# Kernel optimization log

Hardware: AMD Instinct MI355X
Metric: run time of the kernel (lower is better)

Reference implementation:

```python
import jax, jax.numpy as jnp
import numpy as np

N = 8192
EPS = 1e-8
RADIUS2 = 0.05 ** 2  # squared neighborhood radius


def setup_inputs() -> dict:
    key = jax.random.key(0)
    ks = jax.random.split(key, 6)
    points = jax.random.uniform(ks[0], (N, 3), dtype=jnp.float32)
    seg_probs = jax.random.uniform(ks[1], (N, 3), dtype=jnp.float32)
    boundary_mask = jax.random.randint(ks[2], (N,), 0, 2) > 0
    head_mask = jax.random.randint(ks[3], (N,), 0, 2) > 0
    pred_mask = jax.random.randint(ks[4], (N,), 0, 2) > 0
    gt_mask = jax.random.randint(ks[5], (N,), 0, 2) > 0
    return {"points": points, "seg_probs": seg_probs,
            "boundary_mask": boundary_mask, "head_mask": head_mask,
            "pred_mask": pred_mask, "gt_mask": gt_mask}


def _ellipsoid_shape_loss(points, mask):
    # masked mean / covariance over head-region points, then eigen ratios
    m = mask.astype(points.dtype)[:, None]  # [N,1]
    n = jnp.sum(m)
    center = jnp.sum(points * m, axis=0) / n
    centered = (points - center) * m  # zero out non-head rows
    cov = centered.T @ centered / n  # [3,3]
    w = jnp.linalg.eigvalsh(cov)  # ascending
    a, b, c = w[2], w[1], w[0]  # descending
    loss = (b / (a + EPS) - 1.0) ** 2 + (c / (a + EPS) - 1.0) ** 2
    return jnp.where(n >= 10, loss, 0.0)


def _size_consistency_loss(pred_mask, gt_mask):
    pv = jnp.sum(pred_mask.astype(jnp.float32))
    gv = jnp.sum(gt_mask.astype(jnp.float32))
    volume_loss = (pv - gv) ** 2
    rel = jnp.abs(pv - gv) / jnp.where(gv > 0, gv, 1.0)
    return jnp.where(gv > 0, volume_loss + 0.5 * rel, volume_loss)


def _surface_smoothness_loss(points, bmask, seg_probs):
    # fused pairwise-distance + masked unbiased variance (replaces O(N) python loop)
    bf = bmask.astype(points.dtype)
    x = seg_probs[:, 2]  # head probability channel
    sq = jnp.sum(points * points, axis=1)  # [N]
    d2 = sq[:, None] + sq[None, :] - 2.0 * (points @ points.T)  # [N,N] squared dists
    vf = (d2 < RADIUS2).astype(points.dtype) * bf[:, None] * bf[None, :]  # valid pairs
    cnt = jnp.sum(vf, axis=1)  # neighbors per boundary point (incl. self)
    sx = vf @ x
    sx2 = vf @ (x * x)
    safe_n = jnp.maximum(cnt, 2.0)
    var = (sx2 - sx * sx / safe_n) / (safe_n - 1.0)  # unbiased, matches torch.var
    include = (cnt > 1.0) & bmask
    ni = jnp.sum(include)
    mean_var = jnp.sum(jnp.where(include, var, 0.0)) / jnp.maximum(ni, 1)
    ok = (jnp.sum(bf) >= 5) & (ni > 0)
    return jnp.where(ok, mean_var, 0.0)


def _connectivity_loss(points, hmask):
    hf = hmask.astype(points.dtype)
    n = jnp.sum(hf)
    center = jnp.sum(points * hf[:, None], axis=0) / n
    d = jnp.linalg.norm(points - center, axis=1)
    mean_d = jnp.sum(d * hf) / n
    var = jnp.sum(hf * (d - mean_d) ** 2) / (n - 1.0)  # unbiased
    maxd = jnp.max(jnp.where(hmask, d, -jnp.inf))
    return jnp.where(n >= 5, var / (maxd + EPS), 0.0)


def reference(points, seg_probs, boundary_mask, head_mask, pred_mask, gt_mask):
    total = (_ellipsoid_shape_loss(points, head_mask)
             + _size_consistency_loss(pred_mask, gt_mask)
             + _surface_smoothness_loss(points, boundary_mask, seg_probs)
             + _connectivity_loss(points, head_mask))
    return total
```

## Files before the change

### kernel.cpp

```cpp
#include <hip/hip_runtime.h>

#define EPSF 1e-8f
#define R2C  0.0025f
#define NJ   32


__device__ inline int read_mask(const void* p, int i, int isInt) {
    if (isInt) return ((const int*)p)[i] != 0;
    return ((const unsigned char*)p)[i] != 0;
}
__device__ inline float wave_sum(float v) {
    #pragma unroll
    for (int o = 32; o > 0; o >>= 1) v += __shfl_down(v, o, 64);
    return v;
}
__device__ inline float wave_max(float v) {
    #pragma unroll
    for (int o = 32; o > 0; o >>= 1) v = fmaxf(v, __shfl_down(v, o, 64));
    return v;
}

__global__ __launch_bounds__(256, 4)
void k_pairs(const float* __restrict__ pts, const float* __restrict__ segp,
             const void* bm, const void* hm, const void* pm, const void* gm,
             float* __restrict__ ws, int n, int nbi) {
    __shared__ float4 t4[256];
    __shared__ float2 tv[256];
    __shared__ int bad[4];
    __shared__ float pacc[8];
    int tid = threadIdx.x, lane = tid & 63;
    int bx = blockIdx.x, c = blockIdx.y;

    if (tid < 4) bad[tid] = 0;
    if (tid < 8) pacc[tid] = 0.f;
    __syncthreads();
    {
        const void* ms[4] = {bm, hm, pm, gm};
        #pragma unroll
        for (int m = 0; m < 4; ++m) {
            unsigned w = ((const unsigned*)ms[m])[tid & 255];
            if (w & 0xFFFFFF00u) atomicOr(&bad[m], 1);
        }
    }
    __syncthreads();

    int i0 = bx*512 + tid, i1 = i0 + 256;
    int ic0 = min(i0, n-1), ic1 = min(i1, n-1);
    bool a0 = i0 < n, a1 = i1 < n;
    float x0 = pts[3*ic0], y0 = pts[3*ic0+1], z0 = pts[3*ic0+2];
    float x1 = pts[3*ic1], y1 = pts[3*ic1+1], z1 = pts[3*ic1+2];
    int b0 = read_mask(bm, ic0, !bad[0]) && a0;
    int b1 = read_mask(bm, ic1, !bad[0]) && a1;
    float thr0 = b0 ? R2C - (x0*x0 + y0*y0 + z0*z0) : -1e30f;
    float thr1 = b1 ? R2C - (x1*x1 + y1*y1 + z1*z1) : -1e30f;

    if (c == 0) {
        int h0 = read_mask(hm, ic0, !bad[1]) && a0;
        int h1 = read_mask(hm, ic1, !bad[1]) && a1;
        int p0 = read_mask(pm, ic0, !bad[2]) && a0;
        int p1 = read_mask(pm, ic1, !bad[2]) && a1;
        int g0 = read_mask(gm, ic0, !bad[3]) && a0;
        int g1 = read_mask(gm, ic1, !bad[3]) && a1;
        float hf0 = h0 ? 1.f : 0.f, hf1 = h1 ? 1.f : 0.f;
        float vals[7] = { hf0*x0 + hf1*x1, hf0*y0 + hf1*y1, hf0*z0 + hf1*z1,
                          hf0 + hf1, (float)(p0 + p1), (float)(g0 + g1),
                          (float)(b0 + b1) };
        #pragma unroll
        for (int k = 0; k < 7; ++k) {
            float s = wave_sum(vals[k]);
            if (lane == 0) atomicAdd(&pacc[k], s);
        }
        __syncthreads();
        if (tid < 7) ws[64 + bx*8 + tid] = pacc[tid];
    }

    {
        int j = c*256 + tid;
        int jc = min(j, n-1);
        bool jact = j < n;
        float xj = pts[3*jc], yj = pts[3*jc+1], zj = pts[3*jc+2];
        int bj = read_mask(bm, jc, !bad[0]) && jact;
        float v = segp[3*jc+2];
        float sqj = xj*xj + yj*yj + zj*zj;
        t4[tid] = make_float4(-2.f*xj, -2.f*yj, -2.f*zj, bj ? sqj : sqj + 1000.f);
        tv[tid] = make_float2(v, v*v);
    }
    __syncthreads();

    float c0a = 0.f, s10 = 0.f, s20 = 0.f;
    float c1a = 0.f, s11 = 0.f, s21 = 0.f;
    #pragma unroll 8
    for (int k = 0; k < 256; ++k) {
        float4 pj = t4[k];
        float2 vv = tv[k];
        float t0 = fmaf(pj.x, x0, pj.w);
        t0 = fmaf(pj.y, y0, t0);
        t0 = fmaf(pj.z, z0, t0);
        float m0 = (t0 < thr0) ? 1.f : 0.f;
        c0a += m0;
        s10 = fmaf(m0, vv.x, s10);
        s20 = fmaf(m0, vv.y, s20);
        float t1 = fmaf(pj.x, x1, pj.w);
        t1 = fmaf(pj.y, y1, t1);
        t1 = fmaf(pj.z, z1, t1);
        float m1 = (t1 < thr1) ? 1.f : 0.f;
        c1a += m1;
        s11 = fmaf(m1, vv.x, s11);
        s21 = fmaf(m1, vv.y, s21);
    }
    float* __restrict__ outb = ws + 4096;
    if (a0) {
        outb[(size_t)c*n + i0]          = c0a;
        outb[(size_t)(NJ + c)*n + i0]   = s10;
        outb[(size_t)(2*NJ + c)*n + i0] = s20;
    }
    if (a1) {
        outb[(size_t)c*n + i1]          = c1a;
        outb[(size_t)(NJ + c)*n + i1]   = s11;
        outb[(size_t)(2*NJ + c)*n + i1] = s21;
    }
}

__global__ void k_final(const float* __restrict__ pts, const void* bm, const void* hm,
                        float* __restrict__ ws, float* __restrict__ out,
                        int n, int nbi, int nsl) {
    __shared__ int badb, badh, lastf, bmax;
    __shared__ float ctr[8];
    __shared__ float bacc[12];
    int tid = threadIdx.x, lane = tid & 63;
    if (tid == 0) { badb = 0; badh = 0; lastf = 0; bmax = 0; }
    if (tid < 12) bacc[tid] = 0.f;
    __syncthreads();
    unsigned wb = ((const unsigned*)bm)[tid & 255];
    unsigned wh = ((const unsigned*)hm)[tid & 255];
    if (wb & 0xFFFFFF00u) atomicOr(&badb, 1);
    if (wh & 0xFFFFFF00u) atomicOr(&badh, 1);

    if (tid < 64) {
        float s[7] = {0.f,0.f,0.f,0.f,0.f,0.f,0.f};
        for (int r = tid; r < nsl; r += 64)
            #pragma unroll
            for (int k = 0; k < 7; ++k) s[k] += ws[64 + r*8 + k];
        #pragma unroll
        for (int k = 0; k < 7; ++k) {
            #pragma unroll
            for (int o = 32; o > 0; o >>= 1) s[k] += __shfl_down(s[k], o, 64);
        }
        if (tid == 0) {
            #pragma unroll
            for (int k = 0; k < 7; ++k) ctr[k] = s[k];
        }
    }
    __syncthreads();

    float nh = ctr[3];
    float inv = (nh > 0.f) ? 1.f/nh : 0.f;
    float cx = ctr[0]*inv, cy = ctr[1]*inv, cz = ctr[2]*inv;
    int i = blockIdx.x*256 + tid;
    int ic = min(i, n-1);
    float act = (i < n) ? 1.f : 0.f;
    float x = pts[3*ic], y = pts[3*ic+1], z = pts[3*ic+2];
    int h = read_mask(hm, ic, !badh);
    float m = (h ? 1.f : 0.f) * act;
    float dx = x-cx, dy = y-cy, dz = z-cz;
    float d = sqrtf(dx*dx + dy*dy + dz*dz);
    float vals[8] = { m*dx*dx, m*dx*dy, m*dx*dz, m*dy*dy, m*dy*dz, m*dz*dz,
                      m*d, m*d*d };
    #pragma unroll
    for (int k = 0; k < 8; ++k) {
        float s = wave_sum(vals[k]);
        if (lane == 0) atomicAdd(&bacc[k], s);
    }
    float dm = wave_max(m > 0.f ? d : 0.f);
    if (lane == 0) atomicMax(&bmax, __float_as_int(dm));

    const float* __restrict__ outb = ws + 4096;
    float sv = 0.f, nv = 0.f;
    if (i < n) {
        float c0 = 0.f, a1 = 0.f, a2 = 0.f;
        #pragma unroll
        for (int k = 0; k < NJ; ++k) {
            c0 += outb[(size_t)k*n + i];
            a1 += outb[(size_t)(NJ + k)*n + i];
            a2 += outb[(size_t)(2*NJ + k)*n + i];
        }
        int b = read_mask(bm, i, !badb);
        float safe_n = fmaxf(c0, 2.f);
        float var = (a2 - a1*a1/safe_n) / (safe_n - 1.f);
        if (b && c0 > 1.f) { sv = var; nv = 1.f; }
    }
    sv = wave_sum(sv); nv = wave_sum(nv);
    if (lane == 0) { atomicAdd(&bacc[9], sv); atomicAdd(&bacc[10], nv); }
    __syncthreads();

    float* row = ws + 1024 + blockIdx.x*16;
    if (tid < 12) {
        float val = (tid == 8) ? __int_as_float(bmax) : bacc[tid];
        atomicExch((int*)&row[tid], __float_as_int(val));
    }
    if (tid == 0) {
        __threadfence();
        unsigned prev = atomicAdd((unsigned*)ws, 1u);
        if (prev % (unsigned)gridDim.x == (unsigned)gridDim.x - 1u) lastf = 1;
    }
    __syncthreads();
    if (!lastf) return;

    if (tid < 12) bacc[tid] = 0.f;
    if (tid == 0) bmax = 0;
    __syncthreads();
    for (int t = tid; t < nbi*12; t += 256) {
        int r = t / 12, col = t % 12;
        int bits = atomicOr((int*)&ws[1024 + r*16 + col], 0);
        if (col == 8) atomicMax(&bmax, bits);
        else          atomicAdd(&bacc[col], __int_as_float(bits));
    }
    __syncthreads();
    if (tid != 0) return;

    float cxx=bacc[0], cxy=bacc[1], cxz=bacc[2];
    float cyy=bacc[3], cyz=bacc[4], czz=bacc[5];
    float sd=bacc[6], sd2=bacc[7], svv=bacc[9], niv=bacc[10];
    float maxd = __int_as_float(bmax);
    float pv = ctr[4], gv = ctr[5], nbm = ctr[6];

    float el = 0.0f;
    if (nh >= 10.0f) {
        double nn  = (double)nh;
        double axx = cxx/nn, axy = cxy/nn, axz = cxz/nn;
        double ayy = cyy/nn, ayz = cyz/nn, azz = czz/nn;
        double p1 = axy*axy + axz*axz + ayz*ayz;
        double q  = (axx + ayy + azz) / 3.0;
        double p2 = (axx-q)*(axx-q) + (ayy-q)*(ayy-q) + (azz-q)*(azz-q) + 2.0*p1;
        double e0, e2;
        if (p2 < 1e-300) { e0 = e2 = q; }
        else {
            double p = sqrt(p2 / 6.0);
            double bxx = (axx-q)/p, byy = (ayy-q)/p, bzz = (azz-q)/p;
            double bxy = axy/p, bxz = axz/p, byz = ayz/p;
            double detB = bxx*(byy*bzz - byz*byz) - bxy*(bxy*bzz - byz*bxz)
                        + bxz*(bxy*byz - byy*bxz);
            double r2 = fmin(1.0, fmax(-1.0, detB * 0.5));
            double phi = acos(r2) / 3.0;
            e2 = q + 2.0*p*cos(phi);
            e0 = q + 2.0*p*cos(phi + 2.0943951023931953);
        }
        double e1 = 3.0*q - e2 - e0;
        double ra = e1/(e2 + (double)EPSF) - 1.0;
        double rc = e0/(e2 + (double)EPSF) - 1.0;
        el = (float)(ra*ra + rc*rc);
    }
    float diff = pv - gv;
    float vol = diff * diff;
    float rel = fabsf(diff) / (gv > 0.0f ? gv : 1.0f);
    float sc = (gv > 0.0f) ? vol + 0.5f*rel : vol;
    float mean_var = svv / fmaxf(niv, 1.0f);
    float ss = ((nbm >= 5.0f) && (niv > 0.0f)) ? mean_var : 0.0f;
    float conn = 0.0f;
    if (nh >= 5.0f) {
        float var = (sd2 - sd*sd/nh) / (nh - 1.0f);
        conn = var / (maxd + EPSF);
    }
    out[0] = el + sc + ss + conn;
}

extern "C" void kernel_launch(void* const* d_in, const int* in_sizes, int n_in,
                              void* d_out, int out_size, void* d_ws, size_t ws_size,
                              hipStream_t stream) {
    const float* points = (const float*)d_in[0];
    const float* segp   = (const float*)d_in[1];
    const void*  bmask  = d_in[2];
    const void*  hmask  = d_in[3];
    const void*  pmask  = d_in[4];
    const void*  gmask  = d_in[5];
    float* ws  = (float*)d_ws;
    float* out = (float*)d_out;
    int n = in_sizes[2];
    int nbi = (n + 255) / 256;
    int nsl = (n + 511) / 512;

    k_pairs<<<dim3(nsl, NJ), 256, 0, stream>>>(points, segp, bmask, hmask,
                                               pmask, gmask, ws, n, nbi);
    k_final<<<nbi, 256, 0, stream>>>(points, bmask, hmask, ws, out, n, nbi, nsl);
}
```

Before: 32.45 us.

## Compact boundary j-points in shared memory and compute covariance from raw moments

Each block now ballot-compacts only the boundary-masked j points into shared memory and loops over that compacted count, skipping roughly half the pairwise work. The covariance is computed from raw second moments gathered in the first kernel, so the final kernel drops six wave reductions. Only the c==0 blocks check the non-boundary masks. The raw-moment covariance in float is less numerically stable, and the loop now has a variable trip count with less unrolling.

```diff
diff --git a/kernel.cpp b/kernel.cpp
--- a/kernel.cpp
+++ b/kernel.cpp
@@ -27,19 +27,24 @@
     __shared__ float4 t4[256];
     __shared__ float2 tv[256];
     __shared__ int bad[4];
-    __shared__ float pacc[8];
-    int tid = threadIdx.x, lane = tid & 63;
+    __shared__ int wc[4];
+    __shared__ float pacc[13];
+    int tid = threadIdx.x, lane = tid & 63, wv = tid >> 6;
     int bx = blockIdx.x, c = blockIdx.y;
 
-    if (tid < 4) bad[tid] = 0;
-    if (tid < 8) pacc[tid] = 0.f;
+    if (tid < 4) { bad[tid] = 0; wc[tid] = 0; }
+    if (tid < 13) pacc[tid] = 0.f;
     __syncthreads();
     {
-        const void* ms[4] = {bm, hm, pm, gm};
-        #pragma unroll
-        for (int m = 0; m < 4; ++m) {
-            unsigned w = ((const unsigned*)ms[m])[tid & 255];
-            if (w & 0xFFFFFF00u) atomicOr(&bad[m], 1);
+        unsigned w0 = ((const unsigned*)bm)[tid & 255];
+        if (w0 & 0xFFFFFF00u) atomicOr(&bad[0], 1);
+        if (c == 0) {
+            unsigned w1 = ((const unsigned*)hm)[tid & 255];
+            unsigned w2 = ((const unsigned*)pm)[tid & 255];
+            unsigned w3 = ((const unsigned*)gm)[tid & 255];
+            if (w1 & 0xFFFFFF00u) atomicOr(&bad[1], 1);
+            if (w2 & 0xFFFFFF00u) atomicOr(&bad[2], 1);
+            if (w3 & 0xFFFFFF00u) atomicOr(&bad[3], 1);
         }
     }
     __syncthreads();
@@ -62,35 +67,47 @@
         int g0 = read_mask(gm, ic0, !bad[3]) && a0;
         int g1 = read_mask(gm, ic1, !bad[3]) && a1;
         float hf0 = h0 ? 1.f : 0.f, hf1 = h1 ? 1.f : 0.f;
-        float vals[7] = { hf0*x0 + hf1*x1, hf0*y0 + hf1*y1, hf0*z0 + hf1*z1,
-                          hf0 + hf1, (float)(p0 + p1), (float)(g0 + g1),
-                          (float)(b0 + b1) };
+        float vals[13] = {
+            hf0*x0 + hf1*x1, hf0*y0 + hf1*y1, hf0*z0 + hf1*z1,
+            hf0 + hf1, (float)(p0 + p1), (float)(g0 + g1), (float)(b0 + b1),
+            hf0*x0*x0 + hf1*x1*x1, hf0*x0*y0 + hf1*x1*y1, hf0*x0*z0 + hf1*x1*z1,
+            hf0*y0*y0 + hf1*y1*y1, hf0*y0*z0 + hf1*y1*z1, hf0*z0*z0 + hf1*z1*z1 };
         #pragma unroll
-        for (int k = 0; k < 7; ++k) {
+        for (int k = 0; k < 13; ++k) {
             float s = wave_sum(vals[k]);
             if (lane == 0) atomicAdd(&pacc[k], s);
         }
         __syncthreads();
-        if (tid < 7) ws[64 + bx*8 + tid] = pacc[tid];
+        if (tid < 13) ws[64 + bx*16 + tid] = pacc[tid];
     }
 
     {
         int j = c*256 + tid;
         int jc = min(j, n-1);
-        bool jact = j < n;
+        bool jb = (j < n) && read_mask(bm, jc, !bad[0]);
         float xj = pts[3*jc], yj = pts[3*jc+1], zj = pts[3*jc+2];
-        int bj = read_mask(bm, jc, !bad[0]) && jact;
         float v = segp[3*jc+2];
         float sqj = xj*xj + yj*yj + zj*zj;
-        t4[tid] = make_float4(-2.f*xj, -2.f*yj, -2.f*zj, bj ? sqj : sqj + 1000.f);
-        tv[tid] = make_float2(v, v*v);
-    }
-    __syncthreads();
+        unsigned long long ball = __ballot(jb);
+        int pre = __popcll(ball & ((1ull << lane) - 1ull));
+        if (lane == 0) wc[wv] = __popcll(ball);
+        __syncthreads();
+        int base = 0;
+        #pragma unroll
+        for (int w = 0; w < 4; ++w) base += (w < wv) ? wc[w] : 0;
+        if (jb) {
+            int r = base + pre;
+            t4[r] = make_float4(-2.f*xj, -2.f*yj, -2.f*zj, sqj);
+            tv[r] = make_float2(v, v*v);
+        }
+    }
+    __syncthreads();
+    int JC = wc[0] + wc[1] + wc[2] + wc[3];
 
     float c0a = 0.f, s10 = 0.f, s20 = 0.f;
     float c1a = 0.f, s11 = 0.f, s21 = 0.f;
-    #pragma unroll 8
-    for (int k = 0; k < 256; ++k) {
+    #pragma unroll 4
+    for (int k = 0; k < JC; ++k) {
         float4 pj = t4[k];
         float2 vv = tv[k];
         float t0 = fmaf(pj.x, x0, pj.w);
@@ -125,11 +142,11 @@
                         float* __restrict__ ws, float* __restrict__ out,
                         int n, int nbi, int nsl) {
     __shared__ int badb, badh, lastf, bmax;
-    __shared__ float ctr[8];
-    __shared__ float bacc[12];
+    __shared__ float ctr[13];
+    __shared__ float bacc[4];
     int tid = threadIdx.x, lane = tid & 63;
     if (tid == 0) { badb = 0; badh = 0; lastf = 0; bmax = 0; }
-    if (tid < 12) bacc[tid] = 0.f;
+    if (tid < 4) bacc[tid] = 0.f;
     __syncthreads();
     unsigned wb = ((const unsigned*)bm)[tid & 255];
     unsigned wh = ((const unsigned*)hm)[tid & 255];
@@ -137,18 +154,19 @@
     if (wh & 0xFFFFFF00u) atomicOr(&badh, 1);
 
     if (tid < 64) {
-        float s[7] = {0.f,0.f,0.f,0.f,0.f,0.f,0.f};
-        for (int r = tid; r < nsl; r += 64)
+        float s[13] = {0,0,0,0,0,0,0,0,0,0,0,0,0};
+        for (int r = tid; r < nsl; r += 64) {
             #pragma unroll
-            for (int k = 0; k < 7; ++k) s[k] += ws[64 + r*8 + k];
+            for (int k = 0; k < 13; ++k) s[k] += ws[64 + r*16 + k];
+        }
         #pragma unroll
-        for (int k = 0; k < 7; ++k) {
+        for (int k = 0; k < 13; ++k) {
             #pragma unroll
             for (int o = 32; o > 0; o >>= 1) s[k] += __shfl_down(s[k], o, 64);
         }
         if (tid == 0) {
             #pragma unroll
-            for (int k = 0; k < 7; ++k) ctr[k] = s[k];
+            for (int k = 0; k < 13; ++k) ctr[k] = s[k];
         }
     }
     __syncthreads();
@@ -164,16 +182,15 @@
     float m = (h ? 1.f : 0.f) * act;
     float dx = x-cx, dy = y-cy, dz = z-cz;
     float d = sqrtf(dx*dx + dy*dy + dz*dz);
-    float vals[8] = { m*dx*dx, m*dx*dy, m*dx*dz, m*dy*dy, m*dy*dz, m*dz*dz,
-                      m*d, m*d*d };
-    #pragma unroll
-    for (int k = 0; k < 8; ++k) {
-        float s = wave_sum(vals[k]);
-        if (lane == 0) atomicAdd(&bacc[k], s);
-    }
-    float dm = wave_max(m > 0.f ? d : 0.f);
-    if (lane == 0) atomicMax(&bmax, __float_as_int(dm));
-
+    {
+        float s0 = wave_sum(m*d);
+        float s1 = wave_sum(m*d*d);
+        float dm = wave_max(m > 0.f ? d : 0.f);
+        if (lane == 0) {
+            atomicAdd(&bacc[0], s0); atomicAdd(&bacc[1], s1);
+            atomicMax(&bmax, __float_as_int(dm));
+        }
+    }
     const float* __restrict__ outb = ws + 4096;
     float sv = 0.f, nv = 0.f;
     if (i < n) {
@@ -190,12 +207,13 @@
         if (b && c0 > 1.f) { sv = var; nv = 1.f; }
     }
     sv = wave_sum(sv); nv = wave_sum(nv);
-    if (lane == 0) { atomicAdd(&bacc[9], sv); atomicAdd(&bacc[10], nv); }
+    if (lane == 0) { atomicAdd(&bacc[2], sv); atomicAdd(&bacc[3], nv); }
     __syncthreads();
 
     float* row = ws + 1024 + blockIdx.x*16;
-    if (tid < 12) {
-        float val = (tid == 8) ? __int_as_float(bmax) : bacc[tid];
+    if (tid < 5) {
+        float val = (tid == 2) ? __int_as_float(bmax)
+                  : (tid < 2 ? bacc[tid] : bacc[tid - 1]);
         atomicExch((int*)&row[tid], __float_as_int(val));
     }
     if (tid == 0) {
@@ -206,29 +224,35 @@
     __syncthreads();
     if (!lastf) return;
 
-    if (tid < 12) bacc[tid] = 0.f;
+    if (tid < 4) bacc[tid] = 0.f;
     if (tid == 0) bmax = 0;
     __syncthreads();
-    for (int t = tid; t < nbi*12; t += 256) {
-        int r = t / 12, col = t % 12;
+    for (int t = tid; t < nbi*5; t += 256) {
+        int r = t / 5, col = t % 5;
         int bits = atomicOr((int*)&ws[1024 + r*16 + col], 0);
-        if (col == 8) atomicMax(&bmax, bits);
-        else          atomicAdd(&bacc[col], __int_as_float(bits));
+        if (col == 2) atomicMax(&bmax, bits);
+        else {
+            int dst = (col < 2) ? col : col - 1;
+            atomicAdd(&bacc[dst], __int_as_float(bits));
+        }
     }
     __syncthreads();
     if (tid != 0) return;
 
-    float cxx=bacc[0], cxy=bacc[1], cxz=bacc[2];
-    float cyy=bacc[3], cyz=bacc[4], czz=bacc[5];
-    float sd=bacc[6], sd2=bacc[7], svv=bacc[9], niv=bacc[10];
+    float sd = bacc[0], sd2 = bacc[1], svv = bacc[2], niv = bacc[3];
     float maxd = __int_as_float(bmax);
     float pv = ctr[4], gv = ctr[5], nbm = ctr[6];
 
     float el = 0.0f;
     if (nh >= 10.0f) {
         double nn  = (double)nh;
-        double axx = cxx/nn, axy = cxy/nn, axz = cxz/nn;
-        double ayy = cyy/nn, ayz = cyz/nn, azz = czz/nn;
+        double cxd = (double)ctr[0]/nn, cyd = (double)ctr[1]/nn, czd = (double)ctr[2]/nn;
+        double axx = (double)ctr[7]/nn  - cxd*cxd;
+        double axy = (double)ctr[8]/nn  - cxd*cyd;
+        double axz = (double)ctr[9]/nn  - cxd*czd;
+        double ayy = (double)ctr[10]/nn - cyd*cyd;
+        double ayz = (double)ctr[11]/nn - cyd*czd;
+        double azz = (double)ctr[12]/nn - czd*czd;
         double p1 = axy*axy + axz*axz + ayz*ayz;
         double q  = (axx + ayy + azz) / 3.0;
         double p2 = (axx-q)*(axx-q) + (ayy-q)*(ayy-q) + (azz-q)*(azz-q) + 2.0*p1;
```

After: 26.10 us (median of 2 runs). -19.6%, faster.
